# Kernel tuning notes

Hardware: AMD Instinct MI355X
Metric: run time of the kernel (lower is better)

Reference implementation:

```python
import jax, jax.numpy as jnp
import numpy as np

D = 1024        # input_dim == hidden_dim (residual add requires equality)
NUM_CLASSES = 2
EPS = 1e-5      # torch LayerNorm default


def _layer_norm(x, gamma, beta):
    mu = jnp.mean(x, axis=-1, keepdims=True)
    var = jnp.var(x, axis=-1, keepdims=True)
    return (x - mu) * jax.lax.rsqrt(var + EPS) * gamma + beta


def setup_inputs() -> dict:
    key = jax.random.key(0)
    ks = jax.random.split(key, 16)
    B, S = 8, 2048
    s = 1.0 / np.sqrt(D)
    inp = {
        "x": jax.random.normal(ks[0], (B, S, D), dtype=jnp.float32),
        "Wq": jax.random.normal(ks[1], (D, D), dtype=jnp.float32) * s,
        "bq": jnp.zeros((D,), jnp.float32),
        "Wk": jax.random.normal(ks[2], (D, D), dtype=jnp.float32) * s,
        "bk": jnp.zeros((D,), jnp.float32),
        "Wv": jax.random.normal(ks[3], (D, D), dtype=jnp.float32) * s,
        "bv": jnp.zeros((D,), jnp.float32),
        "Wd": jax.random.normal(ks[4], (D, D), dtype=jnp.float32) * s,
        "bd": jnp.zeros((D,), jnp.float32),
        "g1": jnp.ones((D,), jnp.float32),
        "b1": jnp.zeros((D,), jnp.float32),
        "g2": jnp.ones((D,), jnp.float32),
        "b2": jnp.zeros((D,), jnp.float32),
        "Wc": jax.random.normal(ks[5], (D, NUM_CLASSES), dtype=jnp.float32) * s,
        "bc": jnp.zeros((NUM_CLASSES,), jnp.float32),
    }
    return inp


def reference(x, Wq, bq, Wk, bk, Wv, bv, Wd, bd, g1, b1, g2, b2, Wc, bc):
    # Q/K/V projections
    q = x @ Wq + bq                                   # [B,S,D]
    k = x @ Wk + bk
    v = x @ Wv + bv
    # scores scaled by sqrt(input_dim) (as in the original code)
    scores = jnp.einsum('bsd,btd->bst', q, k) / np.sqrt(D).astype(np.float32)
    attn = jax.nn.softmax(scores, axis=-1)            # [B,S,S]
    weighted = jnp.einsum('bst,btd->bsd', attn, v)    # [B,S,D]
    weighted = _layer_norm(weighted + x, g1, b1)
    h = jax.nn.relu(weighted @ Wd + bd)
    h = _layer_norm(h + weighted, g2, b2)
    # dropout is identity in eval mode
    logits = h[:, 0, :] @ Wc + bc                     # [B,num_classes]
    return logits
```

## Files before the change

### kernel.cpp

```cpp
#include <hip/hip_runtime.h>
#include <math.h>

#define B 8
#define S 2048
#define D 1024

__device__ __forceinline__ float waveReduceSum(float v) {
#pragma unroll
    for (int k = 32; k >= 1; k >>= 1) v += __shfl_xor(v, k, 64);
    return v;
}
__device__ __forceinline__ float waveReduceMax(float v) {
#pragma unroll
    for (int k = 32; k >= 1; k >>= 1) v = fmaxf(v, __shfl_xor(v, k, 64));
    return v;
}
__device__ float blockReduceSum(float v) {
    __shared__ float sm[4];
    int lane = threadIdx.x & 63, wid = threadIdx.x >> 6;
    v = waveReduceSum(v);
    __syncthreads();
    if (lane == 0) sm[wid] = v;
    __syncthreads();
    return sm[0] + sm[1] + sm[2] + sm[3];
}

__global__ void __launch_bounds__(256) k1_q0(const float* __restrict__ x,
                                             const float* __restrict__ Wq,
                                             const float* __restrict__ bq,
                                             float* __restrict__ q0,
                                             float* __restrict__ zero_region) {
    const int tid = threadIdx.x;
    zero_region[blockIdx.x * 256 + tid] = 0.f;

    const int dp0 = blockIdx.x * 16;
    const int dpl = tid & 15, kg = tid >> 4;
    __shared__ float xs[8][1024];
    for (int j = tid; j < 2048; j += 256) {
        int b = j >> 8, off = j & 255;
        ((float4*)xs[b])[off] = ((const float4*)(x + (size_t)b * S * D))[off];
    }
    __syncthreads();
    float acc[8] = {0.f, 0.f, 0.f, 0.f, 0.f, 0.f, 0.f, 0.f};
    const int k0 = kg * 64;
    for (int i = 0; i < 64; ++i) {
        int k = k0 + i;
        float wv = Wq[(size_t)k * D + dp0 + dpl];
#pragma unroll
        for (int b = 0; b < 8; ++b) acc[b] += xs[b][k] * wv;
    }
    __shared__ float red[16 * 16 * 9];
#pragma unroll
    for (int b = 0; b < 8; ++b) red[(kg * 16 + dpl) * 9 + b] = acc[b];
    __syncthreads();
    if (tid < 128) {
        int dpl2 = tid >> 3, b = tid & 7;
        float s = 0.f;
#pragma unroll
        for (int g = 0; g < 16; ++g) s += red[(g * 16 + dpl2) * 9 + b];
        q0[b * D + dp0 + dpl2] = s + bq[dp0 + dpl2];
    }
}

__global__ void __launch_bounds__(256) k2_u(const float* __restrict__ Wk,
                                            const float* __restrict__ q0,
                                            float* __restrict__ u) {
    int wid = (blockIdx.x * 256 + threadIdx.x) >> 6;
    int lane = threadIdx.x & 63;
    const float4* Wk4 = (const float4*)(Wk + (size_t)wid * D);
    const float4* q04 = (const float4*)q0;
    float acc[8] = {0.f, 0.f, 0.f, 0.f, 0.f, 0.f, 0.f, 0.f};
#pragma unroll
    for (int i = 0; i < 4; ++i) {
        float4 wv = Wk4[lane + 64 * i];
#pragma unroll
        for (int b = 0; b < 8; ++b) {
            float4 qv = q04[b * 256 + lane + 64 * i];
            acc[b] += wv.x * qv.x + wv.y * qv.y + wv.z * qv.z + wv.w * qv.w;
        }
    }
#pragma unroll
    for (int b = 0; b < 8; ++b) {
        float v = waveReduceSum(acc[b]);
        if (lane == 0) u[b * D + wid] = v;
    }
}

__global__ void __launch_bounds__(256) k3_attn(const float* __restrict__ x,
                                               const float* __restrict__ u,
                                               float* __restrict__ pml,
                                               float* __restrict__ pw) {
    const int b = blockIdx.y;
    const int t0 = blockIdx.x * 16;
    const int tid = threadIdx.x;
    const int wave = tid >> 6, lane = tid & 63;
    const float4* xb4 = (const float4*)(x + (size_t)b * S * D);
    float4 xr[16];
#pragma unroll
    for (int t = 0; t < 16; ++t) xr[t] = xb4[(size_t)(t0 + t) * 256 + tid];
    float4 uv = ((const float4*)(u + b * D))[tid];
    __shared__ float part[16][256];
#pragma unroll
    for (int t = 0; t < 16; ++t)
        part[t][tid] = xr[t].x * uv.x + xr[t].y * uv.y + xr[t].z * uv.z + xr[t].w * uv.w;
    __syncthreads();
    __shared__ float s_sc[16];
#pragma unroll
    for (int r = 0; r < 4; ++r) {
        int t = wave * 4 + r;
        float v = part[t][lane] + part[t][lane + 64] + part[t][lane + 128] + part[t][lane + 192];
        v = waveReduceSum(v);
        if (lane == 0) s_sc[t] = v * 0.03125f;
    }
    __syncthreads();
    float m = -INFINITY;
#pragma unroll
    for (int t = 0; t < 16; ++t) m = fmaxf(m, s_sc[t]);
    float p[16], l = 0.f;
#pragma unroll
    for (int t = 0; t < 16; ++t) {
        p[t] = __expf(s_sc[t] - m);
        l += p[t];
    }
    float4 wl = {0.f, 0.f, 0.f, 0.f};
#pragma unroll
    for (int t = 0; t < 16; ++t) {
        wl.x += p[t] * xr[t].x;
        wl.y += p[t] * xr[t].y;
        wl.z += p[t] * xr[t].z;
        wl.w += p[t] * xr[t].w;
    }
    const int pidx = b * 128 + blockIdx.x;
    ((float4*)(pw + (size_t)pidx * 1024))[tid] = wl;
    if (tid == 0) {
        pml[pidx * 2 + 0] = m;
        pml[pidx * 2 + 1] = l;
    }
}

__global__ void __launch_bounds__(256) k4_comb_wv(const float* __restrict__ pml,
                                                  const float* __restrict__ pw,
                                                  const float* __restrict__ Wv,
                                                  float* __restrict__ wacc) {
    const int tid = threadIdx.x;
    const int bid = blockIdx.x;
    const int d0 = (bid >> 2) * 32;
    const int dp = (bid & 3) * 256 + tid;
    const int wave = tid >> 6, lane = tid & 63;
    __shared__ float pm[8][128], pl[8][128], sc[8][128];
    __shared__ float sM[8], sL[8];
    __shared__ float vs[8][32];
    for (int j = tid; j < 1024; j += 256) {
        int b = j >> 7, blk = j & 127;
        pm[b][blk] = pml[(b * 128 + blk) * 2 + 0];
        pl[b][blk] = pml[(b * 128 + blk) * 2 + 1];
    }
    __syncthreads();
#pragma unroll
    for (int h = 0; h < 2; ++h) {
        int b = wave + h * 4;
        float mv = fmaxf(pm[b][lane], pm[b][lane + 64]);
        float M = waveReduceMax(mv);
        float lp = __expf(pm[b][lane] - M) * pl[b][lane] +
                   __expf(pm[b][lane + 64] - M) * pl[b][lane + 64];
        float L = waveReduceSum(lp);
        if (lane == 0) {
            sM[b] = M;
            sL[b] = L;
        }
    }
    __syncthreads();
    for (int j = tid; j < 1024; j += 256) {
        int b = j >> 7, blk = j & 127;
        sc[b][blk] = __expf(pm[b][blk] - sM[b]);
    }
    __syncthreads();
    {
        int b = tid >> 5, dd = tid & 31, d = d0 + dd;
        float acc = 0.f;
#pragma unroll 4
        for (int blk = 0; blk < 128; ++blk)
            acc += sc[b][blk] * pw[(size_t)(b * 128 + blk) * 1024 + d];
        vs[b][dd] = acc / sL[b];
    }
    __syncthreads();
    float acc[8] = {0.f, 0.f, 0.f, 0.f, 0.f, 0.f, 0.f, 0.f};
#pragma unroll 4
    for (int dd = 0; dd < 32; ++dd) {
        float wv = Wv[(size_t)(d0 + dd) * D + dp];
#pragma unroll
        for (int b = 0; b < 8; ++b) acc[b] += vs[b][dd] * wv;
    }
#pragma unroll
    for (int b = 0; b < 8; ++b) atomicAdd(&wacc[b * D + dp], acc[b]);
}

__global__ void __launch_bounds__(256) k5_ln1_wd(const float* __restrict__ wacc,
                                                 const float* __restrict__ bv,
                                                 const float* __restrict__ x,
                                                 const float* __restrict__ g1,
                                                 const float* __restrict__ b1,
                                                 const float* __restrict__ Wd,
                                                 float* __restrict__ hacc) {
    const int tid = threadIdx.x;
    const int bid = blockIdx.x;
    const int d0 = (bid >> 2) * 32;
    const int dp = (bid & 3) * 256 + tid;
    __shared__ float sMu[8], sInv[8], vs[8][32];
    for (int b = 0; b < 8; ++b) {
        float s = 0.f, ss = 0.f;
#pragma unroll
        for (int i = 0; i < 4; ++i) {
            int e = tid * 4 + i;
            float v = wacc[b * D + e] + bv[e] + x[(size_t)b * S * D + e];
            s += v;
            ss += v * v;
        }
        s = blockReduceSum(s);
        ss = blockReduceSum(ss);
        if (tid == 0) {
            float mu = s * (1.0f / D);
            sMu[b] = mu;
            sInv[b] = rsqrtf(ss * (1.0f / D) - mu * mu + 1e-5f);
        }
    }
    __syncthreads();
    {
        int b = tid >> 5, dd = tid & 31, d = d0 + dd;
        float v = wacc[b * D + d] + bv[d] + x[(size_t)b * S * D + d];
        vs[b][dd] = (v - sMu[b]) * sInv[b] * g1[d] + b1[d];
    }
    __syncthreads();
    float acc[8] = {0.f, 0.f, 0.f, 0.f, 0.f, 0.f, 0.f, 0.f};
#pragma unroll 4
    for (int dd = 0; dd < 32; ++dd) {
        float wv = Wd[(size_t)(d0 + dd) * D + dp];
#pragma unroll
        for (int b = 0; b < 8; ++b) acc[b] += vs[b][dd] * wv;
    }
#pragma unroll
    for (int b = 0; b < 8; ++b) atomicAdd(&hacc[b * D + dp], acc[b]);
}

__global__ void __launch_bounds__(256) k6_final(const float* __restrict__ wacc,
                                                const float* __restrict__ bv,
                                                const float* __restrict__ x,
                                                const float* __restrict__ g1,
                                                const float* __restrict__ b1,
                                                const float* __restrict__ hacc,
                                                const float* __restrict__ bd,
                                                const float* __restrict__ g2,
                                                const float* __restrict__ b2,
                                                const float* __restrict__ Wc,
                                                const float* __restrict__ bc,
                                                float* __restrict__ out) {
    const int b = blockIdx.x;
    const int tid = threadIdx.x;
    float r[4];
    float s = 0.f, ss = 0.f;
#pragma unroll
    for (int i = 0; i < 4; ++i) {
        int e = tid * 4 + i;
        float v = wacc[b * D + e] + bv[e] + x[(size_t)b * S * D + e];
        r[i] = v;
        s += v;
        ss += v * v;
    }
    s = blockReduceSum(s);
    ss = blockReduceSum(ss);
    float mu1 = s * (1.0f / D);
    float inv1 = rsqrtf(ss * (1.0f / D) - mu1 * mu1 + 1e-5f);
    float t[4];
    float s2 = 0.f, ss2 = 0.f;
#pragma unroll
    for (int i = 0; i < 4; ++i) {
        int e = tid * 4 + i;
        float ln1v = (r[i] - mu1) * inv1 * g1[e] + b1[e];
        float h = fmaxf(hacc[b * D + e] + bd[e], 0.f) + ln1v;
        t[i] = h;
        s2 += h;
        ss2 += h * h;
    }
    s2 = blockReduceSum(s2);
    ss2 = blockReduceSum(ss2);
    float mu2 = s2 * (1.0f / D);
    float inv2 = rsqrtf(ss2 * (1.0f / D) - mu2 * mu2 + 1e-5f);
    float p0 = 0.f, p1 = 0.f;
#pragma unroll
    for (int i = 0; i < 4; ++i) {
        int e = tid * 4 + i;
        float l2 = (t[i] - mu2) * inv2 * g2[e] + b2[e];
        p0 += l2 * Wc[e * 2 + 0];
        p1 += l2 * Wc[e * 2 + 1];
    }
    p0 = blockReduceSum(p0);
    p1 = blockReduceSum(p1);
    if (tid == 0) {
        out[b * 2 + 0] = p0 + bc[0];
        out[b * 2 + 1] = p1 + bc[1];
    }
}

extern "C" void kernel_launch(void* const* d_in, const int* in_sizes, int n_in,
                              void* d_out, int out_size, void* d_ws, size_t ws_size,
                              hipStream_t stream) {
    const float* x  = (const float*)d_in[0];
    const float* Wq = (const float*)d_in[1];
    const float* bq = (const float*)d_in[2];
    const float* Wk = (const float*)d_in[3];
    const float* Wv = (const float*)d_in[5];
    const float* bv = (const float*)d_in[6];
    const float* Wd = (const float*)d_in[7];
    const float* bd = (const float*)d_in[8];
    const float* g1 = (const float*)d_in[9];
    const float* b1 = (const float*)d_in[10];
    const float* g2 = (const float*)d_in[11];
    const float* b2 = (const float*)d_in[12];
    const float* Wc = (const float*)d_in[13];
    const float* bc = (const float*)d_in[14];
    float* out = (float*)d_out;

    float* ws   = (float*)d_ws;
    float* q0   = ws;
    float* u    = ws + 8192;
    float* wacc = ws + 16384;
    float* hacc = ws + 24576;
    float* pml  = ws + 32768;
    float* pw   = ws + 34816;

    k1_q0<<<64, 256, 0, stream>>>(x, Wq, bq, q0, wacc);
    k2_u<<<256, 256, 0, stream>>>(Wk, q0, u);
    k3_attn<<<dim3(128, 8), 256, 0, stream>>>(x, u, pml, pw);
    k4_comb_wv<<<128, 256, 0, stream>>>(pml, pw, Wv, wacc);
    k5_ln1_wd<<<128, 256, 0, stream>>>(wacc, bv, x, g1, b1, Wd, hacc);
    k6_final<<<8, 256, 0, stream>>>(wacc, bv, x, g1, b1, hacc, bd, g2, b2, Wc, bc, out);
}
```

Before: 172.2 us.

## Fuse the six kernels into three using software grid barriers

Merges the q0 projection and the Wk·q0 product into one 128-block kernel, and merges the Wv combine, the LN1 plus Wd step and the final LN2 plus classifier into another. Both fused kernels use a flag-based grid barrier placed in workspace. The goal is to cut kernel launch gaps and inter-kernel drain time between the small serial stages. The barrier flags are never reset between calls, so on repeated calls the first barrier can pass before q0 is rewritten. It also relies on all 128 blocks being resident at the same time.

New measurement: 237.8 us. 38.1% more time.

```diff
diff --git a/kernel.cpp b/kernel.cpp
--- a/kernel.cpp
+++ b/kernel.cpp
@@ -25,64 +25,93 @@
     return sm[0] + sm[1] + sm[2] + sm[3];
 }
 
-__global__ void __launch_bounds__(256) k1_q0(const float* __restrict__ x,
-                                             const float* __restrict__ Wq,
-                                             const float* __restrict__ bq,
-                                             float* __restrict__ q0,
-                                             float* __restrict__ zero_region) {
+__device__ __forceinline__ void gridBarrier128(unsigned* flags, unsigned magic) {
+    __syncthreads();
+    __threadfence();
+    if (threadIdx.x == 0)
+        __hip_atomic_store(&flags[blockIdx.x], magic, __ATOMIC_RELEASE, __HIP_MEMORY_SCOPE_AGENT);
+    if (threadIdx.x < 128) {
+        while (__hip_atomic_load(&flags[threadIdx.x], __ATOMIC_ACQUIRE,
+                                 __HIP_MEMORY_SCOPE_AGENT) != magic)
+            __builtin_amdgcn_s_sleep(1);
+    }
+    __syncthreads();
+    __threadfence();
+}
+
+__global__ void __launch_bounds__(256) kA(const float* __restrict__ x,
+                                          const float* __restrict__ Wq,
+                                          const float* __restrict__ bq,
+                                          const float* __restrict__ Wk,
+                                          float* __restrict__ q0,
+                                          float* __restrict__ u,
+                                          float* __restrict__ zero_region,
+                                          unsigned* __restrict__ flagsA) {
     const int tid = threadIdx.x;
-    zero_region[blockIdx.x * 256 + tid] = 0.f;
-
-    const int dp0 = blockIdx.x * 16;
-    const int dpl = tid & 15, kg = tid >> 4;
+    const int bid = blockIdx.x;
+    if (tid < 128) zero_region[bid * 128 + tid] = 0.f;
+
     __shared__ float xs[8][1024];
-    for (int j = tid; j < 2048; j += 256) {
-        int b = j >> 8, off = j & 255;
-        ((float4*)xs[b])[off] = ((const float4*)(x + (size_t)b * S * D))[off];
-    }
-    __syncthreads();
-    float acc[8] = {0.f, 0.f, 0.f, 0.f, 0.f, 0.f, 0.f, 0.f};
-    const int k0 = kg * 64;
-    for (int i = 0; i < 64; ++i) {
-        int k = k0 + i;
-        float wv = Wq[(size_t)k * D + dp0 + dpl];
-#pragma unroll
-        for (int b = 0; b < 8; ++b) acc[b] += xs[b][k] * wv;
-    }
     __shared__ float red[16 * 16 * 9];
-#pragma unroll
-    for (int b = 0; b < 8; ++b) red[(kg * 16 + dpl) * 9 + b] = acc[b];
-    __syncthreads();
-    if (tid < 128) {
-        int dpl2 = tid >> 3, b = tid & 7;
-        float s = 0.f;
-#pragma unroll
-        for (int g = 0; g < 16; ++g) s += red[(g * 16 + dpl2) * 9 + b];
-        q0[b * D + dp0 + dpl2] = s + bq[dp0 + dpl2];
-    }
-}
-
-__global__ void __launch_bounds__(256) k2_u(const float* __restrict__ Wk,
-                                            const float* __restrict__ q0,
-                                            float* __restrict__ u) {
-    int wid = (blockIdx.x * 256 + threadIdx.x) >> 6;
-    int lane = threadIdx.x & 63;
-    const float4* Wk4 = (const float4*)(Wk + (size_t)wid * D);
-    const float4* q04 = (const float4*)q0;
-    float acc[8] = {0.f, 0.f, 0.f, 0.f, 0.f, 0.f, 0.f, 0.f};
-#pragma unroll
-    for (int i = 0; i < 4; ++i) {
-        float4 wv = Wk4[lane + 64 * i];
+
+    if (bid < 64) {
+        const int dp0 = bid * 16;
+        const int dpl = tid & 15, kg = tid >> 4;
+        for (int j = tid; j < 2048; j += 256) {
+            int b = j >> 8, off = j & 255;
+            ((float4*)xs[b])[off] = ((const float4*)(x + (size_t)b * S * D))[off];
+        }
+        __syncthreads();
+        float acc[8] = {0.f, 0.f, 0.f, 0.f, 0.f, 0.f, 0.f, 0.f};
+        const int k0 = kg * 64;
+        for (int i = 0; i < 64; ++i) {
+            int k = k0 + i;
+            float wv = Wq[(size_t)k * D + dp0 + dpl];
+#pragma unroll
+            for (int b = 0; b < 8; ++b) acc[b] += xs[b][k] * wv;
+        }
+#pragma unroll
+        for (int b = 0; b < 8; ++b) red[(kg * 16 + dpl) * 9 + b] = acc[b];
+        __syncthreads();
+        if (tid < 128) {
+            int dpl2 = tid >> 3, b = tid & 7;
+            float s = 0.f;
+#pragma unroll
+            for (int g = 0; g < 16; ++g) s += red[(g * 16 + dpl2) * 9 + b];
+            q0[b * D + dp0 + dpl2] = s + bq[dp0 + dpl2];
+        }
+    }
+
+    gridBarrier128(flagsA, 1u);
+
+    {
+        const int wave = tid >> 6, lane = tid & 63;
+        const int r0 = bid * 8 + wave * 2;
+        const float4* W0 = (const float4*)(Wk + (size_t)r0 * D);
+        const float4* W1 = (const float4*)(Wk + (size_t)(r0 + 1) * D);
+        const float4* q04 = (const float4*)q0;
+        float a0[8] = {0.f, 0.f, 0.f, 0.f, 0.f, 0.f, 0.f, 0.f};
+        float a1[8] = {0.f, 0.f, 0.f, 0.f, 0.f, 0.f, 0.f, 0.f};
+#pragma unroll
+        for (int i = 0; i < 4; ++i) {
+            float4 w0 = W0[lane + 64 * i];
+            float4 w1 = W1[lane + 64 * i];
+#pragma unroll
+            for (int b = 0; b < 8; ++b) {
+                float4 qv = q04[b * 256 + lane + 64 * i];
+                a0[b] += w0.x * qv.x + w0.y * qv.y + w0.z * qv.z + w0.w * qv.w;
+                a1[b] += w1.x * qv.x + w1.y * qv.y + w1.z * qv.z + w1.w * qv.w;
+            }
+        }
 #pragma unroll
         for (int b = 0; b < 8; ++b) {
-            float4 qv = q04[b * 256 + lane + 64 * i];
-            acc[b] += wv.x * qv.x + wv.y * qv.y + wv.z * qv.z + wv.w * qv.w;
-        }
-    }
-#pragma unroll
-    for (int b = 0; b < 8; ++b) {
-        float v = waveReduceSum(acc[b]);
-        if (lane == 0) u[b * D + wid] = v;
+            float v0 = waveReduceSum(a0[b]);
+            float v1 = waveReduceSum(a1[b]);
+            if (lane == 0) {
+                u[b * D + r0] = v0;
+                u[b * D + r0 + 1] = v1;
+            }
+        }
     }
 }
 
@@ -138,10 +167,23 @@
     }
 }
 
-__global__ void __launch_bounds__(256) k4_comb_wv(const float* __restrict__ pml,
-                                                  const float* __restrict__ pw,
-                                                  const float* __restrict__ Wv,
-                                                  float* __restrict__ wacc) {
+__global__ void __launch_bounds__(256) kC(const float* __restrict__ pml,
+                                          const float* __restrict__ pw,
+                                          const float* __restrict__ Wv,
+                                          const float* __restrict__ bv,
+                                          const float* __restrict__ x,
+                                          const float* __restrict__ g1,
+                                          const float* __restrict__ b1,
+                                          const float* __restrict__ Wd,
+                                          const float* __restrict__ bd,
+                                          const float* __restrict__ g2,
+                                          const float* __restrict__ b2,
+                                          const float* __restrict__ Wc,
+                                          const float* __restrict__ bc,
+                                          float* __restrict__ wacc,
+                                          float* __restrict__ hacc,
+                                          unsigned* __restrict__ flagsC,
+                                          float* __restrict__ out) {
     const int tid = threadIdx.x;
     const int bid = blockIdx.x;
     const int d0 = (bid >> 2) * 32;
@@ -150,6 +192,8 @@
     __shared__ float pm[8][128], pl[8][128], sc[8][128];
     __shared__ float sM[8], sL[8];
     __shared__ float vs[8][32];
+    __shared__ float sMu[8], sInv[8];
+
     for (int j = tid; j < 1024; j += 256) {
         int b = j >> 7, blk = j & 127;
         pm[b][blk] = pml[(b * 128 + blk) * 2 + 0];
@@ -184,29 +228,20 @@
         vs[b][dd] = acc / sL[b];
     }
     __syncthreads();
-    float acc[8] = {0.f, 0.f, 0.f, 0.f, 0.f, 0.f, 0.f, 0.f};
+    {
+        float acc[8] = {0.f, 0.f, 0.f, 0.f, 0.f, 0.f, 0.f, 0.f};
 #pragma unroll 4
-    for (int dd = 0; dd < 32; ++dd) {
-        float wv = Wv[(size_t)(d0 + dd) * D + dp];
-#pragma unroll
-        for (int b = 0; b < 8; ++b) acc[b] += vs[b][dd] * wv;
-    }
-#pragma unroll
-    for (int b = 0; b < 8; ++b) atomicAdd(&wacc[b * D + dp], acc[b]);
-}
-
-__global__ void __launch_bounds__(256) k5_ln1_wd(const float* __restrict__ wacc,
-                                                 const float* __restrict__ bv,
-                                                 const float* __restrict__ x,
-                                                 const float* __restrict__ g1,
-                                                 const float* __restrict__ b1,
-                                                 const float* __restrict__ Wd,
-                                                 float* __restrict__ hacc) {
-    const int tid = threadIdx.x;
-    const int bid = blockIdx.x;
-    const int d0 = (bid >> 2) * 32;
-    const int dp = (bid & 3) * 256 + tid;
-    __shared__ float sMu[8], sInv[8], vs[8][32];
+        for (int dd = 0; dd < 32; ++dd) {
+            float wv = Wv[(size_t)(d0 + dd) * D + dp];
+#pragma unroll
+            for (int b = 0; b < 8; ++b) acc[b] += vs[b][dd] * wv;
+        }
+#pragma unroll
+        for (int b = 0; b < 8; ++b) atomicAdd(&wacc[b * D + dp], acc[b]);
+    }
+
+    gridBarrier128(flagsC, 1u);
+
     for (int b = 0; b < 8; ++b) {
         float s = 0.f, ss = 0.f;
 #pragma unroll
@@ -231,73 +266,65 @@
         vs[b][dd] = (v - sMu[b]) * sInv[b] * g1[d] + b1[d];
     }
     __syncthreads();
-    float acc[8] = {0.f, 0.f, 0.f, 0.f, 0.f, 0.f, 0.f, 0.f};
+    {
+        float acc[8] = {0.f, 0.f, 0.f, 0.f, 0.f, 0.f, 0.f, 0.f};
 #pragma unroll 4
-    for (int dd = 0; dd < 32; ++dd) {
-        float wv = Wd[(size_t)(d0 + dd) * D + dp];
-#pragma unroll
-        for (int b = 0; b < 8; ++b) acc[b] += vs[b][dd] * wv;
-    }
-#pragma unroll
-    for (int b = 0; b < 8; ++b) atomicAdd(&hacc[b * D + dp], acc[b]);
-}
-
-__global__ void __launch_bounds__(256) k6_final(const float* __restrict__ wacc,
-                                                const float* __restrict__ bv,
-                                                const float* __restrict__ x,
-                                                const float* __restrict__ g1,
-                                                const float* __restrict__ b1,
-                                                const float* __restrict__ hacc,
-                                                const float* __restrict__ bd,
-                                                const float* __restrict__ g2,
-                                                const float* __restrict__ b2,
-                                                const float* __restrict__ Wc,
-                                                const float* __restrict__ bc,
-                                                float* __restrict__ out) {
-    const int b = blockIdx.x;
-    const int tid = threadIdx.x;
-    float r[4];
-    float s = 0.f, ss = 0.f;
-#pragma unroll
-    for (int i = 0; i < 4; ++i) {
-        int e = tid * 4 + i;
-        float v = wacc[b * D + e] + bv[e] + x[(size_t)b * S * D + e];
-        r[i] = v;
-        s += v;
-        ss += v * v;
-    }
-    s = blockReduceSum(s);
-    ss = blockReduceSum(ss);
-    float mu1 = s * (1.0f / D);
-    float inv1 = rsqrtf(ss * (1.0f / D) - mu1 * mu1 + 1e-5f);
-    float t[4];
-    float s2 = 0.f, ss2 = 0.f;
-#pragma unroll
-    for (int i = 0; i < 4; ++i) {
-        int e = tid * 4 + i;
-        float ln1v = (r[i] - mu1) * inv1 * g1[e] + b1[e];
-        float h = fmaxf(hacc[b * D + e] + bd[e], 0.f) + ln1v;
-        t[i] = h;
-        s2 += h;
-        ss2 += h * h;
-    }
-    s2 = blockReduceSum(s2);
-    ss2 = blockReduceSum(ss2);
-    float mu2 = s2 * (1.0f / D);
-    float inv2 = rsqrtf(ss2 * (1.0f / D) - mu2 * mu2 + 1e-5f);
-    float p0 = 0.f, p1 = 0.f;
-#pragma unroll
-    for (int i = 0; i < 4; ++i) {
-        int e = tid * 4 + i;
-        float l2 = (t[i] - mu2) * inv2 * g2[e] + b2[e];
-        p0 += l2 * Wc[e * 2 + 0];
-        p1 += l2 * Wc[e * 2 + 1];
-    }
-    p0 = blockReduceSum(p0);
-    p1 = blockReduceSum(p1);
-    if (tid == 0) {
-        out[b * 2 + 0] = p0 + bc[0];
-        out[b * 2 + 1] = p1 + bc[1];
+        for (int dd = 0; dd < 32; ++dd) {
+            float wv = Wd[(size_t)(d0 + dd) * D + dp];
+#pragma unroll
+            for (int b = 0; b < 8; ++b) acc[b] += vs[b][dd] * wv;
+        }
+#pragma unroll
+        for (int b = 0; b < 8; ++b) atomicAdd(&hacc[b * D + dp], acc[b]);
+    }
+
+    gridBarrier128(flagsC, 2u);
+
+    if (bid < 8) {
+        const int b = bid;
+        float r[4];
+        float s = 0.f, ss = 0.f;
+#pragma unroll
+        for (int i = 0; i < 4; ++i) {
+            int e = tid * 4 + i;
+            float v = wacc[b * D + e] + bv[e] + x[(size_t)b * S * D + e];
+            r[i] = v;
+            s += v;
+            ss += v * v;
+        }
+        s = blockReduceSum(s);
+        ss = blockReduceSum(ss);
+        float mu1 = s * (1.0f / D);
+        float inv1 = rsqrtf(ss * (1.0f / D) - mu1 * mu1 + 1e-5f);
+        float t[4];
+        float s2 = 0.f, ss2 = 0.f;
+#pragma unroll
+        for (int i = 0; i < 4; ++i) {
+            int e = tid * 4 + i;
+            float ln1v = (r[i] - mu1) * inv1 * g1[e] + b1[e];
+            float h = fmaxf(hacc[b * D + e] + bd[e], 0.f) + ln1v;
+            t[i] = h;
+            s2 += h;
+            ss2 += h * h;
+        }
+        s2 = blockReduceSum(s2);
+        ss2 = blockReduceSum(ss2);
+        float mu2 = s2 * (1.0f / D);
+        float inv2 = rsqrtf(ss2 * (1.0f / D) - mu2 * mu2 + 1e-5f);
+        float p0 = 0.f, p1 = 0.f;
+#pragma unroll
+        for (int i = 0; i < 4; ++i) {
+            int e = tid * 4 + i;
+            float l2 = (t[i] - mu2) * inv2 * g2[e] + b2[e];
+            p0 += l2 * Wc[e * 2 + 0];
+            p1 += l2 * Wc[e * 2 + 1];
+        }
+        p0 = blockReduceSum(p0);
+        p1 = blockReduceSum(p1);
+        if (tid == 0) {
+            out[b * 2 + 0] = p0 + bc[0];
+            out[b * 2 + 1] = p1 + bc[1];
+        }
     }
 }
 
@@ -327,11 +354,11 @@
     float* hacc = ws + 24576;
     float* pml  = ws + 32768;
     float* pw   = ws + 34816;
-
-    k1_q0<<<64, 256, 0, stream>>>(x, Wq, bq, q0, wacc);
-    k2_u<<<256, 256, 0, stream>>>(Wk, q0, u);
+    unsigned* flagsA = (unsigned*)(ws + 34816 + 1048576);
+    unsigned* flagsC = flagsA + 128;
+
+    kA<<<128, 256, 0, stream>>>(x, Wq, bq, Wk, q0, u, wacc, flagsA);
     k3_attn<<<dim3(128, 8), 256, 0, stream>>>(x, u, pml, pw);
-    k4_comb_wv<<<128, 256, 0, stream>>>(pml, pw, Wv, wacc);
-    k5_ln1_wd<<<128, 256, 0, stream>>>(wacc, bv, x, g1, b1, Wd, hacc);
-    k6_final<<<8, 256, 0, stream>>>(wacc, bv, x, g1, b1, hacc, bd, g2, b2, Wc, bc, out);
-}
+    kC<<<128, 256, 0, stream>>>(pml, pw, Wv, bv, x, g1, b1, Wd, bd, g2, b2, Wc, bc,
+                                wacc, hacc, flagsC, out);
+}
```
